# Kernel optimization log

Measured on AMD Instinct MI355X. Metric: run time of the kernel, lower is better.

Reference implementation:

```python
import jax, jax.numpy as jnp
import numpy as np

# Dims per init_kwargs
B, C_IN, H, W = 64, 512, 28, 28
GROWTH, BN_SIZE = 32, 4
C_MID = BN_SIZE * GROWTH  # 128
EPS = 1e-5
NUM_BITS = 8          # activation & weight quantization bits
NUM_CHUNKS = 16       # RangeBN chunking (eladhoffer quantize.py default)


def quantize(x, num_bits):
    """Uniform min/max quantize-dequantize (UniformQuantize forward)."""
    mn = x.min()
    mx = x.max()
    qmax = 2.0 ** num_bits - 1.0
    scale = jnp.maximum((mx - mn) / qmax, 1e-8)
    q = jnp.round((jnp.clip(x, mn, mx) - mn) / scale)
    return q * scale + mn


def conv2d(x, w, pad):
    return jax.lax.conv_general_dilated(
        x, w, window_strides=(1, 1), padding=[(pad, pad), (pad, pad)],
        dimension_numbers=('NCHW', 'OIHW', 'NCHW'))


def batchnorm2d(x, w, b):
    # training-mode BN: batch statistics over (N,H,W), biased variance
    mean = x.mean(axis=(0, 2, 3), keepdims=True)
    var = x.var(axis=(0, 2, 3), keepdims=True)
    xhat = (x - mean) * jax.lax.rsqrt(var + EPS)
    return xhat * w.reshape(1, -1, 1, 1) + b.reshape(1, -1, 1, 1)


def range_bn(x, w, b):
    # Range-based BN (training-mode): per-channel mean, scale from chunked min/max range
    Bx, Cx, Hx, Wx = x.shape
    y = x.transpose(1, 0, 2, 3).reshape(Cx, NUM_CHUNKS, -1)  # [C, chunks, n]
    mean_max = y.max(-1).mean(-1)   # [C]
    mean_min = y.min(-1).mean(-1)   # [C]
    mean = y.reshape(Cx, -1).mean(-1)  # [C]
    n = y.shape[-1]
    scale_fix = (0.5 * 0.35) * (1.0 + (np.pi * np.log(4.0)) ** 0.5) / ((2.0 * np.log(float(n))) ** 0.5)
    scale = 1.0 / ((mean_max - mean_min) * scale_fix + EPS)
    out = (x - mean.reshape(1, Cx, 1, 1)) * scale.reshape(1, Cx, 1, 1)
    qw = quantize(w, NUM_BITS)
    qb = quantize(b, NUM_BITS)
    return out * qw.reshape(1, Cx, 1, 1) + qb.reshape(1, Cx, 1, 1)


def setup_inputs() -> dict:
    key = jax.random.key(0)
    ks = jax.random.split(key, 7)
    x = jax.random.normal(ks[0], (B, C_IN, H, W), dtype=jnp.float32)
    bn1_w = jax.random.uniform(ks[1], (C_IN,), dtype=jnp.float32, minval=0.5, maxval=1.5)
    bn1_b = jax.random.normal(ks[2], (C_IN,), dtype=jnp.float32) * 0.1
    conv1_w = jax.random.normal(ks[3], (C_MID, C_IN, 1, 1), dtype=jnp.float32) * (2.0 / C_IN) ** 0.5
    rbn_w = jax.random.uniform(ks[4], (C_MID,), dtype=jnp.float32, minval=0.5, maxval=1.5)
    rbn_b = jax.random.normal(ks[5], (C_MID,), dtype=jnp.float32) * 0.1
    conv2_w = jax.random.normal(ks[6], (GROWTH, C_MID, 3, 3), dtype=jnp.float32) * (2.0 / (9 * C_MID)) ** 0.5
    return {"x": x, "bn1_w": bn1_w, "bn1_b": bn1_b, "conv1_w": conv1_w,
            "rbn_w": rbn_w, "rbn_b": rbn_b, "conv2_w": conv2_w}


def reference(x, bn1_w, bn1_b, conv1_w, rbn_w, rbn_b, conv2_w):
    # norm1 -> relu1 -> QConv2d(1x1) -> RangeBN -> relu2 -> QConv2d(3x3) -> concat
    h = jax.nn.relu(batchnorm2d(x, bn1_w, bn1_b))
    h = conv2d(quantize(h, NUM_BITS), quantize(conv1_w, NUM_BITS), pad=0)
    h = jax.nn.relu(range_bn(h, rbn_w, rbn_b))
    h = conv2d(quantize(h, NUM_BITS), quantize(conv2_w, NUM_BITS), pad=1)
    # drop_rate = 0 -> dropout is identity
    return jnp.concatenate([x, h], axis=1)
```

## Files before the change

kernel.cpp:

```cpp
#include <hip/hip_runtime.h>
#include <math.h>

static constexpr int BB    = 64;
static constexpr int C_IN  = 512;
static constexpr int C_MID = 128;
static constexpr int C_OUT = 32;
static constexpr int C_TOT = 544;
static constexpr int HW    = 784;

static constexpr size_t H2_OFF    = 0;
static constexpr size_t QW1_OFF   = 6422528;
static constexpr size_t QW2_OFF   = QW1_OFF + 65536;
static constexpr size_t PSTAT_OFF = QW2_OFF + 49152;
static constexpr size_t BNA_OFF   = PSTAT_OFF + 16384;
static constexpr size_t BNB_OFF   = BNA_OFF + 512;
static constexpr size_t A2_OFF    = BNB_OFF + 512;
static constexpr size_t B2_OFF    = A2_OFF + 128;
static constexpr size_t QRW_OFF   = B2_OFF + 128;
static constexpr size_t QRB_OFF   = QRW_OFF + 128;
static constexpr size_t SCAL_OFF  = QRB_OFF + 128;
static constexpr size_t ACELL_OFF = SCAL_OFF + 16;
static constexpr size_t RP_OFF    = ACELL_OFF + 112;

#define DEVFN __device__ __forceinline__

typedef __bf16 bf16x8 __attribute__((ext_vector_type(8)));
typedef float  f32x4  __attribute__((ext_vector_type(4)));

DEVFN float qact(float v, float mn, float mx, float inv, float sc) {
    v = fminf(fmaxf(v, mn), mx);
    return fmaf(rintf((v - mn) * inv), sc, mn);
}

DEVFN unsigned f2bf(float f) {
    unsigned u = __float_as_uint(f);
    return (u + 0x7fffu + ((u >> 16) & 1u)) >> 16;
}

DEVFN unsigned fkey(float f) {
    const unsigned u = __float_as_uint(f);
    return (u & 0x80000000u) ? ~u : (u | 0x80000000u);
}
DEVFN float funkey(unsigned k) {
    const unsigned u = (k & 0x80000000u) ? (k & 0x7FFFFFFFu) : ~k;
    return __uint_as_float(u);
}

__global__ void k_init(float* __restrict__ ws) {
    unsigned* cells = (unsigned*)(ws + ACELL_OFF);
    const int t = threadIdx.x;
    if (t < 3) cells[t] = 0xFFFFFFFFu;
    else if (t < 6) cells[4 + (t - 3)] = 0u;
}

__global__ __launch_bounds__(256) void k_stats(const float* __restrict__ x,
                                               const float* __restrict__ conv1_w,
                                               const float* __restrict__ conv2_w,
                                               float* __restrict__ ws) {
    const int bid = blockIdx.x, tid = threadIdx.x;
    __shared__ float r0[256], r1[256], r2[256], r3[256];

    if (bid < 4096) {
        const int c = bid >> 3, bg = bid & 7;
        float s = 0.f, s2 = 0.f, mn = INFINITY, mx = -INFINITY;
        if (tid < 224) {
#pragma unroll
            for (int k = 0; k < 7; ++k) {
                const int idx = k * 224 + tid;
                const int b = bg * 8 + idx / 196, j = idx % 196;
                const float4 v = ((const float4*)(x + ((size_t)b * C_IN + c) * HW))[j];
                s  += (v.x + v.y) + (v.z + v.w);
                s2 += v.x * v.x + v.y * v.y + v.z * v.z + v.w * v.w;
                mn = fminf(mn, fminf(fminf(v.x, v.y), fminf(v.z, v.w)));
                mx = fmaxf(mx, fmaxf(fmaxf(v.x, v.y), fmaxf(v.z, v.w)));
            }
        }
        r0[tid] = s; r1[tid] = s2; r2[tid] = mn; r3[tid] = mx;
        __syncthreads();
        for (int off = 128; off > 0; off >>= 1) {
            if (tid < off) {
                r0[tid] += r0[tid + off];
                r1[tid] += r1[tid + off];
                r2[tid] = fminf(r2[tid], r2[tid + off]);
                r3[tid] = fmaxf(r3[tid], r3[tid + off]);
            }
            __syncthreads();
        }
        if (tid == 0) {
            float* p = ws + PSTAT_OFF + ((size_t)c * 8 + bg) * 4;
            p[0] = r0[0]; p[1] = r1[0]; p[2] = r2[0]; p[3] = r3[0];
        }
    } else {
        float mn = INFINITY, mx = -INFINITY;
        if (bid < 4128) {
            const float4* src = (const float4*)conv1_w + (size_t)(bid - 4096) * 512;
            for (int i = tid; i < 512; i += 256) {
                const float4 v = src[i];
                mn = fminf(mn, fminf(fminf(v.x, v.y), fminf(v.z, v.w)));
                mx = fmaxf(mx, fmaxf(fmaxf(v.x, v.y), fmaxf(v.z, v.w)));
            }
        } else {
            const float4* src = (const float4*)conv2_w + (size_t)(bid - 4128) * 1152;
            for (int i = tid; i < 1152; i += 256) {
                const float4 v = src[i];
                mn = fminf(mn, fminf(fminf(v.x, v.y), fminf(v.z, v.w)));
                mx = fmaxf(mx, fmaxf(fmaxf(v.x, v.y), fmaxf(v.z, v.w)));
            }
        }
        r2[tid] = mn; r3[tid] = mx;
        __syncthreads();
        for (int off = 128; off > 0; off >>= 1) {
            if (tid < off) { r2[tid] = fminf(r2[tid], r2[tid + off]); r3[tid] = fmaxf(r3[tid], r3[tid + off]); }
            __syncthreads();
        }
        if (tid == 0) {
            unsigned* cells = (unsigned*)(ws + ACELL_OFF);
            const int w = (bid < 4128) ? 0 : 1;
            atomicMin(&cells[w],     fkey(r2[0]));
            atomicMax(&cells[4 + w], fkey(r3[0]));
        }
    }
}

__global__ __launch_bounds__(256) void k_prep(const float* __restrict__ conv1_w,
                                              const float* __restrict__ conv2_w,
                                              const float* __restrict__ bn1_w,
                                              const float* __restrict__ bn1_b,
                                              const float* __restrict__ rbn_w,
                                              const float* __restrict__ rbn_b,
                                              float* __restrict__ ws) {
    const int b = blockIdx.x, tid = threadIdx.x;
    const unsigned* cells = (const unsigned*)(ws + ACELL_OFF);
    __shared__ float ra[256], rb[256];
    __shared__ float s_mn, s_sc;

    if (b < 32) {
        const float mnw = funkey(cells[0]), mxw = funkey(cells[4]);
        const float scw = fmaxf((mxw - mnw) / 255.f, 1e-8f);
        unsigned short* qw = (unsigned short*)(ws + QW1_OFF);
        const int base = b * 2048;
#pragma unroll
        for (int t = 0; t < 8; ++t) {
            const int i = base + t * 256 + tid;
            const int co = i >> 9, k = i & 511;
            const float v = conv1_w[i];
            const float qv = fmaf(rintf((v - mnw) / scw), scw, mnw);
            const int ks = k >> 6, kc = (k >> 3) & 7, klo = k & 7;
            qw[(((size_t)ks * 128 + co) << 6) + (((kc ^ (co & 7)) << 3) | klo)] = (unsigned short)f2bf(qv);
        }
    } else if (b < 40) {
        const float mnw = funkey(cells[1]), mxw = funkey(cells[5]);
        const float scw = fmaxf((mxw - mnw) / 255.f, 1e-8f);
        unsigned short* qw2 = (unsigned short*)(ws + QW2_OFF);
        const int base = (b - 32) * 4608;
        for (int i2 = tid; i2 < 4608; i2 += 256) {
            const int i = base + i2;
            const int co = i / 1152, r = i % 1152, ci = r / 9, tap = r % 9;
            const float v = conv2_w[i];
            const float qv = fmaf(rintf((v - mnw) / scw), scw, mnw);
            qw2[(size_t)co * 1152 + tap * 128 + ci] = (unsigned short)f2bf(qv);
        }
    } else if (b == 40) {
        float lmn = INFINITY, lmx = -INFINITY;
        for (int c = tid; c < 512; c += 256) {
            const float* p = ws + PSTAT_OFF + (size_t)c * 32;
            float s = 0.f, s2 = 0.f, cmn = INFINITY, cmx = -INFINITY;
            for (int g = 0; g < 8; ++g) {
                s += p[g * 4 + 0]; s2 += p[g * 4 + 1];
                cmn = fminf(cmn, p[g * 4 + 2]); cmx = fmaxf(cmx, p[g * 4 + 3]);
            }
            const float n = 50176.f;
            const float mean = s / n;
            const float var  = s2 / n - mean * mean;
            const float rstd = rsqrtf(var + 1e-5f);
            const float A  = rstd * bn1_w[c];
            const float Bc = bn1_b[c] - mean * A;
            ws[BNA_OFF + c] = A; ws[BNB_OFF + c] = Bc;
            const float v1 = A * cmn + Bc, v2 = A * cmx + Bc;
            lmn = fminf(lmn, fmaxf(0.f, fminf(v1, v2)));
            lmx = fmaxf(lmx, fmaxf(0.f, fmaxf(v1, v2)));
        }
        ra[tid] = lmn; rb[tid] = lmx;
        __syncthreads();
        for (int off = 128; off > 0; off >>= 1) {
            if (tid < off) { ra[tid] = fminf(ra[tid], ra[tid + off]); rb[tid] = fmaxf(rb[tid], rb[tid + off]); }
            __syncthreads();
        }
        if (tid == 0) {
            const float mn1 = ra[0], mx1 = rb[0];
            const float sc = fmaxf((mx1 - mn1) / 255.f, 1e-8f);
            ws[SCAL_OFF + 0] = mn1; ws[SCAL_OFF + 1] = sc; ws[SCAL_OFF + 2] = 1.f / sc; ws[SCAL_OFF + 6] = mx1;
        }
    } else {
        for (int which = 0; which < 2; ++which) {
            const float* src = which ? rbn_b : rbn_w;
            const size_t dst = which ? QRB_OFF : QRW_OFF;
            float v = 0.f;
            ra[tid] = INFINITY; rb[tid] = -INFINITY;
            if (tid < 128) { v = src[tid]; ra[tid] = v; rb[tid] = v; }
            __syncthreads();
            for (int off = 128; off > 0; off >>= 1) {
                if (tid < off) { ra[tid] = fminf(ra[tid], ra[tid + off]); rb[tid] = fmaxf(rb[tid], rb[tid + off]); }
                __syncthreads();
            }
            if (tid == 0) { s_mn = ra[0]; s_sc = fmaxf((rb[0] - ra[0]) / 255.f, 1e-8f); }
            __syncthreads();
            if (tid < 128) ws[dst + tid] = fmaf(rintf((v - s_mn) / s_sc), s_sc, s_mn);
            __syncthreads();
        }
    }
}

__global__ __launch_bounds__(256, 2) void k_conv1(const float* __restrict__ x,
                                                  float* __restrict__ out,
                                                  float* __restrict__ ws) {
    __shared__ __align__(16) unsigned short wt[128 * 64];
    __shared__ __align__(16) unsigned short ht[112 * 64];
    const int tid = threadIdx.x;
    const int pt = blockIdx.x, b = blockIdx.y;
    const int p0 = pt * 112;
    const float mn1 = ws[SCAL_OFF + 0], sc1 = ws[SCAL_OFF + 1];
    const float inv1 = ws[SCAL_OFF + 2], mx1 = ws[SCAL_OFF + 6];
    const unsigned short* qw1 = (const unsigned short*)(ws + QW1_OFF);
    const float* xb = x + (size_t)b * C_IN * HW;
    float* outb = out + (size_t)b * C_TOT * HW;

    const int o = tid & 7, q = tid >> 3;
    const int wv = tid >> 6, g = (tid >> 4) & 3, r4 = tid & 15;

    f32x4 acc[2][7];
#pragma unroll
    for (int i = 0; i < 2; ++i)
#pragma unroll
        for (int j = 0; j < 7; ++j) acc[i][j] = f32x4{0.f, 0.f, 0.f, 0.f};

    for (int ks = 0; ks < 8; ++ks) {
        const float4* wsrc = (const float4*)(qw1 + (size_t)ks * 8192);
        float4* wdst = (float4*)wt;
#pragma unroll
        for (int i = 0; i < 4; ++i) wdst[tid + i * 256] = wsrc[tid + i * 256];

        if (tid < 224) {
            const int ci0 = ks * 64 + o * 8;
            float vv[8][4];
#pragma unroll
            for (int j = 0; j < 8; ++j) {
                const f32x4 v = *(const f32x4*)(xb + (size_t)(ci0 + j) * HW + p0 + q * 4);
                __builtin_nontemporal_store(v, (f32x4*)(outb + (size_t)(ci0 + j) * HW + p0 + q * 4));
                const float A = ws[BNA_OFF + ci0 + j], Bc = ws[BNB_OFF + ci0 + j];
                vv[j][0] = qact(fmaxf(0.f, fmaf(v.x, A, Bc)), mn1, mx1, inv1, sc1);
                vv[j][1] = qact(fmaxf(0.f, fmaf(v.y, A, Bc)), mn1, mx1, inv1, sc1);
                vv[j][2] = qact(fmaxf(0.f, fmaf(v.z, A, Bc)), mn1, mx1, inv1, sc1);
                vv[j][3] = qact(fmaxf(0.f, fmaf(v.w, A, Bc)), mn1, mx1, inv1, sc1);
            }
#pragma unroll
            for (int r = 0; r < 4; ++r) {
                const int p = q * 4 + r;
                uint4 pk;
                pk.x = f2bf(vv[0][r]) | (f2bf(vv[1][r]) << 16);
                pk.y = f2bf(vv[2][r]) | (f2bf(vv[3][r]) << 16);
                pk.z = f2bf(vv[4][r]) | (f2bf(vv[5][r]) << 16);
                pk.w = f2bf(vv[6][r]) | (f2bf(vv[7][r]) << 16);
                *(uint4*)&ht[p * 64 + ((o ^ (p & 7)) << 3)] = pk;
            }
        }
        __syncthreads();

#pragma unroll
        for (int ksub = 0; ksub < 2; ++ksub) {
            const int kk = ksub * 4 + g;
            bf16x8 af[2], bfr[7];
#pragma unroll
            for (int ct = 0; ct < 2; ++ct) {
                const int co = wv * 32 + ct * 16 + r4;
                af[ct] = *(const bf16x8*)&wt[co * 64 + ((kk ^ (co & 7)) << 3)];
            }
#pragma unroll
            for (int pf = 0; pf < 7; ++pf) {
                const int p = pf * 16 + r4;
                bfr[pf] = *(const bf16x8*)&ht[p * 64 + ((kk ^ (p & 7)) << 3)];
            }
#pragma unroll
            for (int ct = 0; ct < 2; ++ct)
#pragma unroll
                for (int pf = 0; pf < 7; ++pf)
                    acc[ct][pf] = __builtin_amdgcn_mfma_f32_16x16x32_bf16(af[ct], bfr[pf], acc[ct][pf], 0, 0, 0);
        }
        __syncthreads();
    }

    float* hb = ws + H2_OFF + (size_t)b * C_MID * HW;
#pragma unroll
    for (int ct = 0; ct < 2; ++ct) {
        const int co0 = wv * 32 + ct * 16 + g * 4;
#pragma unroll
        for (int pf = 0; pf < 7; ++pf) {
            const int p = p0 + pf * 16 + r4;
#pragma unroll
            for (int r = 0; r < 4; ++r)
                hb[(size_t)(co0 + r) * HW + p] = acc[ct][pf][r];
        }
    }

#pragma unroll
    for (int ct = 0; ct < 2; ++ct)
#pragma unroll
        for (int r = 0; r < 4; ++r) {
            float s = 0.f, mn = INFINITY, mx = -INFINITY;
#pragma unroll
            for (int pf = 0; pf < 7; ++pf) {
                const float v = acc[ct][pf][r];
                s += v; mn = fminf(mn, v); mx = fmaxf(mx, v);
            }
#pragma unroll
            for (int m = 1; m < 16; m <<= 1) {
                s  += __shfl_xor(s, m, 64);
                mn  = fminf(mn, __shfl_xor(mn, m, 64));
                mx  = fmaxf(mx, __shfl_xor(mx, m, 64));
            }
            if (r4 == 0) {
                const int co = wv * 32 + ct * 16 + g * 4 + r;
                float* dst = ws + RP_OFF + (((size_t)co * 64 + b) * 7 + pt) * 3;
                dst[0] = s; dst[1] = mn; dst[2] = mx;
            }
        }
}

__global__ __launch_bounds__(64) void k_rbn_combine(float* __restrict__ ws) {
    const int c = blockIdx.x, t = threadIdx.x;
    const int ch = t >> 2, sub = t & 3;
    const int b = ch * 4 + sub;
    const float* rp = ws + RP_OFF + ((size_t)c * 64 + b) * 21;
    float s = 0.f, mn = INFINITY, mx = -INFINITY;
#pragma unroll
    for (int pt = 0; pt < 7; ++pt) {
        s += rp[pt * 3 + 0];
        mn = fminf(mn, rp[pt * 3 + 1]);
        mx = fmaxf(mx, rp[pt * 3 + 2]);
    }
#pragma unroll
    for (int m = 1; m < 4; m <<= 1) {
        s  += __shfl_xor(s, m, 64);
        mn  = fminf(mn, __shfl_xor(mn, m, 64));
        mx  = fmaxf(mx, __shfl_xor(mx, m, 64));
    }
    float smx = mx, smn = mn, stot = s, gmn = mn, gmx = mx;
#pragma unroll
    for (int m = 4; m < 64; m <<= 1) {
        smx  += __shfl_xor(smx, m, 64);
        smn  += __shfl_xor(smn, m, 64);
        stot += __shfl_xor(stot, m, 64);
        gmn   = fminf(gmn, __shfl_xor(gmn, m, 64));
        gmx   = fmaxf(gmx, __shfl_xor(gmx, m, 64));
    }
    if (t == 0) {
        const float mm = smx * (1.f / 16.f), mnm = smn * (1.f / 16.f);
        const float mean = stot / 50176.f;
        const double PI_D = 3.14159265358979323846;
        const double sfd = 0.175 * (1.0 + sqrt(PI_D * log(4.0))) / sqrt(2.0 * log(3136.0));
        const float scale = 1.f / ((mm - mnm) * (float)sfd + 1e-5f);
        const float A  = scale * ws[QRW_OFF + c];
        const float Bc = ws[QRB_OFF + c] - mean * A;
        ws[A2_OFF + c] = A; ws[B2_OFF + c] = Bc;
        const float v1 = A * gmn + Bc, v2 = A * gmx + Bc;
        const float lo = fmaxf(0.f, fminf(v1, v2));
        const float hi = fmaxf(0.f, fmaxf(v1, v2));
        unsigned* cells = (unsigned*)(ws + ACELL_OFF);
        atomicMin(&cells[2], __float_as_uint(lo));
        atomicMax(&cells[6], __float_as_uint(hi));
    }
}

__global__ __launch_bounds__(128) void k_conv2(float* __restrict__ out, const float* __restrict__ ws) {
    __shared__ __align__(16) unsigned short lact[7 * 30 * 128];
    const int tid = threadIdx.x;
    const int pt = blockIdx.x, b = blockIdx.y;
    const int y0 = pt * 4;
    const unsigned* cells = (const unsigned*)(ws + ACELL_OFF);
    const float mn3 = __uint_as_float(cells[2]);
    const float mx3 = __uint_as_float(cells[6]);
    const float sc3 = fmaxf((mx3 - mn3) / 255.f, 1e-8f);
    const float inv3 = 1.f / sc3;

    {
        const uint4 z = {0u, 0u, 0u, 0u};
        uint4* lp = (uint4*)lact;
        for (int i = tid; i < 3360; i += 128) lp[i] = z;
    }
    __syncthreads();

    const float* h2b = ws + H2_OFF + (size_t)b * C_MID * HW;
    for (int task = tid; task < 672; task += 128) {
        const int oct = task / 42, rem = task % 42, r = rem / 7, xq = rem % 7;
        const int gy = y0 - 1 + r;
        if (gy < 0 || gy > 27) continue;
        float vv[8][4];
#pragma unroll
        for (int j = 0; j < 8; ++j) {
            const int ci = oct * 8 + j;
            const float4 v = *(const float4*)(h2b + (size_t)ci * HW + gy * 28 + xq * 4);
            const float A = ws[A2_OFF + ci], Bc = ws[B2_OFF + ci];
            vv[j][0] = qact(fmaxf(0.f, fmaf(v.x, A, Bc)), mn3, mx3, inv3, sc3);
            vv[j][1] = qact(fmaxf(0.f, fmaf(v.y, A, Bc)), mn3, mx3, inv3, sc3);
            vv[j][2] = qact(fmaxf(0.f, fmaf(v.z, A, Bc)), mn3, mx3, inv3, sc3);
            vv[j][3] = qact(fmaxf(0.f, fmaf(v.w, A, Bc)), mn3, mx3, inv3, sc3);
        }
#pragma unroll
        for (int xi = 0; xi < 4; ++xi) {
            const int col = xq * 4 + xi + 1;
            const int phys = (oct + col) & 15;
            uint4 pk;
            pk.x = f2bf(vv[0][xi]) | (f2bf(vv[1][xi]) << 16);
            pk.y = f2bf(vv[2][xi]) | (f2bf(vv[3][xi]) << 16);
            pk.z = f2bf(vv[4][xi]) | (f2bf(vv[5][xi]) << 16);
            pk.w = f2bf(vv[6][xi]) | (f2bf(vv[7][xi]) << 16);
            *(uint4*)&lact[((r * 30 + col) * 16 + phys) * 8] = pk;
        }
    }
    __syncthreads();

    const int wv = tid >> 6, lane = tid & 63, r4 = lane & 15, g = lane >> 4;
    int py[4], px[4];
#pragma unroll
    for (int i = 0; i < 4; ++i) {
        const int p = (wv * 4 + i) * 16 + r4;
        py[i] = p / 28; px[i] = p % 28;
    }
    f32x4 acc[2][4];
#pragma unroll
    for (int ct = 0; ct < 2; ++ct)
#pragma unroll
        for (int i = 0; i < 4; ++i) acc[ct][i] = f32x4{0.f, 0.f, 0.f, 0.f};

    const unsigned short* qw2 = (const unsigned short*)(ws + QW2_OFF);
    for (int tap = 0; tap < 9; ++tap) {
        const int dy = tap / 3, dx = tap % 3;
        bf16x8 afr[2][4];
#pragma unroll
        for (int ct = 0; ct < 2; ++ct)
#pragma unroll
            for (int c4 = 0; c4 < 4; ++c4) {
                const int co = ct * 16 + r4;
                afr[ct][c4] = *(const bf16x8*)&qw2[(size_t)co * 1152 + tap * 128 + c4 * 32 + g * 8];
            }
#pragma unroll
        for (int c4 = 0; c4 < 4; ++c4) {
            bf16x8 bfr[4];
#pragma unroll
            for (int i = 0; i < 4; ++i) {
                const int row = py[i] + dy, col = px[i] + dx;
                const int phys = (c4 * 4 + g + col) & 15;
                bfr[i] = *(const bf16x8*)&lact[((row * 30 + col) * 16 + phys) * 8];
            }
#pragma unroll
            for (int ct = 0; ct < 2; ++ct)
#pragma unroll
                for (int i = 0; i < 4; ++i)
                    acc[ct][i] = __builtin_amdgcn_mfma_f32_16x16x32_bf16(afr[ct][c4], bfr[i], acc[ct][i], 0, 0, 0);
        }
    }

#pragma unroll
    for (int ct = 0; ct < 2; ++ct)
#pragma unroll
        for (int i = 0; i < 4; ++i) {
            const int pf = wv * 4 + i;
            if (pf < 7) {
                const int p = pf * 16 + r4;
#pragma unroll
                for (int r = 0; r < 4; ++r) {
                    const int co = ct * 16 + g * 4 + r;
                    out[((size_t)b * C_TOT + 512 + co) * HW + y0 * 28 + p] = acc[ct][i][r];
                }
            }
        }
}

extern "C" void kernel_launch(void* const* d_in, const int* in_sizes, int n_in,
                              void* d_out, int out_size, void* d_ws, size_t ws_size,
                              hipStream_t stream) {
    const float* x       = (const float*)d_in[0];
    const float* bn1_w   = (const float*)d_in[1];
    const float* bn1_b   = (const float*)d_in[2];
    const float* conv1_w = (const float*)d_in[3];
    const float* rbn_w   = (const float*)d_in[4];
    const float* rbn_b   = (const float*)d_in[5];
    const float* conv2_w = (const float*)d_in[6];
    float* out = (float*)d_out;
    float* ws  = (float*)d_ws;

    k_init<<<1, 64, 0, stream>>>(ws);
    k_stats<<<4136, 256, 0, stream>>>(x, conv1_w, conv2_w, ws);
    k_prep<<<42, 256, 0, stream>>>(conv1_w, conv2_w, bn1_w, bn1_b, rbn_w, rbn_b, ws);
    k_conv1<<<dim3(7, 64), 256, 0, stream>>>(x, out, ws);
    k_rbn_combine<<<128, 64, 0, stream>>>(ws);
    k_conv2<<<dim3(7, 64), 128, 0, stream>>>(out, ws);
}
```

Baseline: 102.2 us.

## Split conv1 over output-channel halves, store h2 as bf16, drop atomics and init kernel

Replaces the atomic min/max cells and the k_init launch with per-block partial results that are reduced inside k_prep and k_conv2. conv1 is split into two blocks per tile, each covering 64 output channels, which gives more blocks and higher occupancy. Each of those blocks stages x and recomputes the BN/quantize of its input, and only one of them writes the x passthrough. The intermediate h2 is stored in bf16 instead of fp32, halving its write and read traffic at some precision cost before RangeBN. conv2 moves to 256 threads with fewer tiles per wave.

```diff
diff --git a/kernel.cpp b/kernel.cpp
--- a/kernel.cpp
+++ b/kernel.cpp
@@ -19,8 +19,9 @@
 static constexpr size_t QRW_OFF   = B2_OFF + 128;
 static constexpr size_t QRB_OFF   = QRW_OFF + 128;
 static constexpr size_t SCAL_OFF  = QRB_OFF + 128;
-static constexpr size_t ACELL_OFF = SCAL_OFF + 16;
-static constexpr size_t RP_OFF    = ACELL_OFF + 112;
+static constexpr size_t PART_OFF  = SCAL_OFF + 16;
+static constexpr size_t RP_OFF    = PART_OFF + 128;
+static constexpr size_t PART2_OFF = RP_OFF + 172032;
 
 #define DEVFN __device__ __forceinline__
 
@@ -37,21 +38,7 @@
     return (u + 0x7fffu + ((u >> 16) & 1u)) >> 16;
 }
 
-DEVFN unsigned fkey(float f) {
-    const unsigned u = __float_as_uint(f);
-    return (u & 0x80000000u) ? ~u : (u | 0x80000000u);
-}
-DEVFN float funkey(unsigned k) {
-    const unsigned u = (k & 0x80000000u) ? (k & 0x7FFFFFFFu) : ~k;
-    return __uint_as_float(u);
-}
-
-__global__ void k_init(float* __restrict__ ws) {
-    unsigned* cells = (unsigned*)(ws + ACELL_OFF);
-    const int t = threadIdx.x;
-    if (t < 3) cells[t] = 0xFFFFFFFFu;
-    else if (t < 6) cells[4 + (t - 3)] = 0u;
-}
+DEVFN float bf2f(unsigned short h) { return __uint_as_float((unsigned)h << 16); }
 
 __global__ __launch_bounds__(256) void k_stats(const float* __restrict__ x,
                                                const float* __restrict__ conv1_w,
@@ -63,17 +50,13 @@
     if (bid < 4096) {
         const int c = bid >> 3, bg = bid & 7;
         float s = 0.f, s2 = 0.f, mn = INFINITY, mx = -INFINITY;
-        if (tid < 224) {
-#pragma unroll
-            for (int k = 0; k < 7; ++k) {
-                const int idx = k * 224 + tid;
-                const int b = bg * 8 + idx / 196, j = idx % 196;
-                const float4 v = ((const float4*)(x + ((size_t)b * C_IN + c) * HW))[j];
-                s  += (v.x + v.y) + (v.z + v.w);
-                s2 += v.x * v.x + v.y * v.y + v.z * v.z + v.w * v.w;
-                mn = fminf(mn, fminf(fminf(v.x, v.y), fminf(v.z, v.w)));
-                mx = fmaxf(mx, fmaxf(fmaxf(v.x, v.y), fmaxf(v.z, v.w)));
-            }
+        for (int i = tid; i < 1568; i += 256) {
+            const int b = bg * 8 + i / 196, j = i % 196;
+            const float4 v = ((const float4*)(x + ((size_t)b * C_IN + c) * HW))[j];
+            s  += (v.x + v.y) + (v.z + v.w);
+            s2 += v.x * v.x + v.y * v.y + v.z * v.z + v.w * v.w;
+            mn = fminf(mn, fminf(fminf(v.x, v.y), fminf(v.z, v.w)));
+            mx = fmaxf(mx, fmaxf(fmaxf(v.x, v.y), fmaxf(v.z, v.w)));
         }
         r0[tid] = s; r1[tid] = s2; r2[tid] = mn; r3[tid] = mx;
         __syncthreads();
@@ -114,10 +97,9 @@
             __syncthreads();
         }
         if (tid == 0) {
-            unsigned* cells = (unsigned*)(ws + ACELL_OFF);
-            const int w = (bid < 4128) ? 0 : 1;
-            atomicMin(&cells[w],     fkey(r2[0]));
-            atomicMax(&cells[4 + w], fkey(r3[0]));
+            float* p = (bid < 4128) ? ws + PART_OFF + (size_t)(bid - 4096) * 2
+                                    : ws + PART_OFF + 64 + (size_t)(bid - 4128) * 2;
+            p[0] = r2[0]; p[1] = r3[0];
         }
     }
 }
@@ -130,13 +112,20 @@
                                               const float* __restrict__ rbn_b,
                                               float* __restrict__ ws) {
     const int b = blockIdx.x, tid = threadIdx.x;
-    const unsigned* cells = (const unsigned*)(ws + ACELL_OFF);
     __shared__ float ra[256], rb[256];
     __shared__ float s_mn, s_sc;
 
     if (b < 32) {
-        const float mnw = funkey(cells[0]), mxw = funkey(cells[4]);
-        const float scw = fmaxf((mxw - mnw) / 255.f, 1e-8f);
+        ra[tid] = tid < 32 ? ws[PART_OFF + tid * 2] : INFINITY;
+        rb[tid] = tid < 32 ? ws[PART_OFF + tid * 2 + 1] : -INFINITY;
+        __syncthreads();
+        for (int off = 128; off > 0; off >>= 1) {
+            if (tid < off) { ra[tid] = fminf(ra[tid], ra[tid + off]); rb[tid] = fmaxf(rb[tid], rb[tid + off]); }
+            __syncthreads();
+        }
+        if (tid == 0) { s_mn = ra[0]; s_sc = fmaxf((rb[0] - ra[0]) / 255.f, 1e-8f); }
+        __syncthreads();
+        const float mnw = s_mn, scw = s_sc;
         unsigned short* qw = (unsigned short*)(ws + QW1_OFF);
         const int base = b * 2048;
 #pragma unroll
@@ -149,8 +138,16 @@
             qw[(((size_t)ks * 128 + co) << 6) + (((kc ^ (co & 7)) << 3) | klo)] = (unsigned short)f2bf(qv);
         }
     } else if (b < 40) {
-        const float mnw = funkey(cells[1]), mxw = funkey(cells[5]);
-        const float scw = fmaxf((mxw - mnw) / 255.f, 1e-8f);
+        ra[tid] = tid < 8 ? ws[PART_OFF + 64 + tid * 2] : INFINITY;
+        rb[tid] = tid < 8 ? ws[PART_OFF + 64 + tid * 2 + 1] : -INFINITY;
+        __syncthreads();
+        for (int off = 128; off > 0; off >>= 1) {
+            if (tid < off) { ra[tid] = fminf(ra[tid], ra[tid + off]); rb[tid] = fmaxf(rb[tid], rb[tid + off]); }
+            __syncthreads();
+        }
+        if (tid == 0) { s_mn = ra[0]; s_sc = fmaxf((rb[0] - ra[0]) / 255.f, 1e-8f); }
+        __syncthreads();
+        const float mnw = s_mn, scw = s_sc;
         unsigned short* qw2 = (unsigned short*)(ws + QW2_OFF);
         const int base = (b - 32) * 4608;
         for (int i2 = tid; i2 < 4608; i2 += 256) {
@@ -211,13 +208,13 @@
     }
 }
 
-__global__ __launch_bounds__(256, 2) void k_conv1(const float* __restrict__ x,
+__global__ __launch_bounds__(256, 3) void k_conv1(const float* __restrict__ x,
                                                   float* __restrict__ out,
                                                   float* __restrict__ ws) {
-    __shared__ __align__(16) unsigned short wt[128 * 64];
+    __shared__ __align__(16) unsigned short wt[64 * 64];
     __shared__ __align__(16) unsigned short ht[112 * 64];
     const int tid = threadIdx.x;
-    const int pt = blockIdx.x, b = blockIdx.y;
+    const int pt = blockIdx.x, b = blockIdx.y, ch = blockIdx.z;
     const int p0 = pt * 112;
     const float mn1 = ws[SCAL_OFF + 0], sc1 = ws[SCAL_OFF + 1];
     const float inv1 = ws[SCAL_OFF + 2], mx1 = ws[SCAL_OFF + 6];
@@ -228,17 +225,15 @@
     const int o = tid & 7, q = tid >> 3;
     const int wv = tid >> 6, g = (tid >> 4) & 3, r4 = tid & 15;
 
-    f32x4 acc[2][7];
-#pragma unroll
-    for (int i = 0; i < 2; ++i)
-#pragma unroll
-        for (int j = 0; j < 7; ++j) acc[i][j] = f32x4{0.f, 0.f, 0.f, 0.f};
+    f32x4 acc[7];
+#pragma unroll
+    for (int j = 0; j < 7; ++j) acc[j] = f32x4{0.f, 0.f, 0.f, 0.f};
 
     for (int ks = 0; ks < 8; ++ks) {
-        const float4* wsrc = (const float4*)(qw1 + (size_t)ks * 8192);
+        const float4* wsrc = (const float4*)(qw1 + (((size_t)ks * 128 + (size_t)ch * 64) << 6));
         float4* wdst = (float4*)wt;
-#pragma unroll
-        for (int i = 0; i < 4; ++i) wdst[tid + i * 256] = wsrc[tid + i * 256];
+        wdst[tid] = wsrc[tid];
+        wdst[tid + 256] = wsrc[tid + 256];
 
         if (tid < 224) {
             const int ci0 = ks * 64 + o * 8;
@@ -246,7 +241,8 @@
 #pragma unroll
             for (int j = 0; j < 8; ++j) {
                 const f32x4 v = *(const f32x4*)(xb + (size_t)(ci0 + j) * HW + p0 + q * 4);
-                __builtin_nontemporal_store(v, (f32x4*)(outb + (size_t)(ci0 + j) * HW + p0 + q * 4));
+                if (ch == 0)
+                    __builtin_nontemporal_store(v, (f32x4*)(outb + (size_t)(ci0 + j) * HW + p0 + q * 4));
                 const float A = ws[BNA_OFF + ci0 + j], Bc = ws[BNB_OFF + ci0 + j];
                 vv[j][0] = qact(fmaxf(0.f, fmaf(v.x, A, Bc)), mn1, mx1, inv1, sc1);
                 vv[j][1] = qact(fmaxf(0.f, fmaf(v.y, A, Bc)), mn1, mx1, inv1, sc1);
@@ -269,61 +265,51 @@
 #pragma unroll
         for (int ksub = 0; ksub < 2; ++ksub) {
             const int kk = ksub * 4 + g;
-            bf16x8 af[2], bfr[7];
-#pragma unroll
-            for (int ct = 0; ct < 2; ++ct) {
-                const int co = wv * 32 + ct * 16 + r4;
-                af[ct] = *(const bf16x8*)&wt[co * 64 + ((kk ^ (co & 7)) << 3)];
-            }
+            const int col = wv * 16 + r4;
+            const bf16x8 af = *(const bf16x8*)&wt[col * 64 + ((kk ^ (col & 7)) << 3)];
+            bf16x8 bfr[7];
 #pragma unroll
             for (int pf = 0; pf < 7; ++pf) {
                 const int p = pf * 16 + r4;
                 bfr[pf] = *(const bf16x8*)&ht[p * 64 + ((kk ^ (p & 7)) << 3)];
             }
 #pragma unroll
-            for (int ct = 0; ct < 2; ++ct)
-#pragma unroll
-                for (int pf = 0; pf < 7; ++pf)
-                    acc[ct][pf] = __builtin_amdgcn_mfma_f32_16x16x32_bf16(af[ct], bfr[pf], acc[ct][pf], 0, 0, 0);
-        }
-        __syncthreads();
-    }
-
-    float* hb = ws + H2_OFF + (size_t)b * C_MID * HW;
-#pragma unroll
-    for (int ct = 0; ct < 2; ++ct) {
-        const int co0 = wv * 32 + ct * 16 + g * 4;
+            for (int pf = 0; pf < 7; ++pf)
+                acc[pf] = __builtin_amdgcn_mfma_f32_16x16x32_bf16(af, bfr[pf], acc[pf], 0, 0, 0);
+        }
+        __syncthreads();
+    }
+
+    unsigned short* hb = (unsigned short*)(ws + H2_OFF) + (size_t)b * C_MID * HW;
+    const int co0 = ch * 64 + wv * 16 + g * 4;
+#pragma unroll
+    for (int pf = 0; pf < 7; ++pf) {
+        const int p = p0 + pf * 16 + r4;
+#pragma unroll
+        for (int r = 0; r < 4; ++r)
+            hb[(size_t)(co0 + r) * HW + p] = (unsigned short)f2bf(acc[pf][r]);
+    }
+
+#pragma unroll
+    for (int r = 0; r < 4; ++r) {
+        float s = 0.f, mn = INFINITY, mx = -INFINITY;
 #pragma unroll
         for (int pf = 0; pf < 7; ++pf) {
-            const int p = p0 + pf * 16 + r4;
-#pragma unroll
-            for (int r = 0; r < 4; ++r)
-                hb[(size_t)(co0 + r) * HW + p] = acc[ct][pf][r];
-        }
-    }
-
-#pragma unroll
-    for (int ct = 0; ct < 2; ++ct)
-#pragma unroll
-        for (int r = 0; r < 4; ++r) {
-            float s = 0.f, mn = INFINITY, mx = -INFINITY;
-#pragma unroll
-            for (int pf = 0; pf < 7; ++pf) {
-                const float v = acc[ct][pf][r];
-                s += v; mn = fminf(mn, v); mx = fmaxf(mx, v);
-            }
-#pragma unroll
-            for (int m = 1; m < 16; m <<= 1) {
-                s  += __shfl_xor(s, m, 64);
-                mn  = fminf(mn, __shfl_xor(mn, m, 64));
-                mx  = fmaxf(mx, __shfl_xor(mx, m, 64));
-            }
-            if (r4 == 0) {
-                const int co = wv * 32 + ct * 16 + g * 4 + r;
-                float* dst = ws + RP_OFF + (((size_t)co * 64 + b) * 7 + pt) * 3;
-                dst[0] = s; dst[1] = mn; dst[2] = mx;
-            }
-        }
+            const float v = acc[pf][r];
+            s += v; mn = fminf(mn, v); mx = fmaxf(mx, v);
+        }
+#pragma unroll
+        for (int m = 1; m < 16; m <<= 1) {
+            s  += __shfl_xor(s, m, 64);
+            mn  = fminf(mn, __shfl_xor(mn, m, 64));
+            mx  = fmaxf(mx, __shfl_xor(mx, m, 64));
+        }
+        if (r4 == 0) {
+            const int co = co0 + r;
+            float* dst = ws + RP_OFF + (((size_t)co * 64 + b) * 7 + pt) * 3;
+            dst[0] = s; dst[1] = mn; dst[2] = mx;
+        }
+    }
 }
 
 __global__ __launch_bounds__(64) void k_rbn_combine(float* __restrict__ ws) {
@@ -363,34 +349,40 @@
         const float Bc = ws[QRB_OFF + c] - mean * A;
         ws[A2_OFF + c] = A; ws[B2_OFF + c] = Bc;
         const float v1 = A * gmn + Bc, v2 = A * gmx + Bc;
-        const float lo = fmaxf(0.f, fminf(v1, v2));
-        const float hi = fmaxf(0.f, fmaxf(v1, v2));
-        unsigned* cells = (unsigned*)(ws + ACELL_OFF);
-        atomicMin(&cells[2], __float_as_uint(lo));
-        atomicMax(&cells[6], __float_as_uint(hi));
-    }
-}
-
-__global__ __launch_bounds__(128) void k_conv2(float* __restrict__ out, const float* __restrict__ ws) {
+        ws[PART2_OFF + c * 2 + 0] = fmaxf(0.f, fminf(v1, v2));
+        ws[PART2_OFF + c * 2 + 1] = fmaxf(0.f, fmaxf(v1, v2));
+    }
+}
+
+__global__ __launch_bounds__(256, 2) void k_conv2(float* __restrict__ out, const float* __restrict__ ws) {
     __shared__ __align__(16) unsigned short lact[7 * 30 * 128];
+    __shared__ float sra[128], srb[128];
+    __shared__ float s_mn3, s_mx3, s_sc3, s_inv3;
     const int tid = threadIdx.x;
     const int pt = blockIdx.x, b = blockIdx.y;
     const int y0 = pt * 4;
-    const unsigned* cells = (const unsigned*)(ws + ACELL_OFF);
-    const float mn3 = __uint_as_float(cells[2]);
-    const float mx3 = __uint_as_float(cells[6]);
-    const float sc3 = fmaxf((mx3 - mn3) / 255.f, 1e-8f);
-    const float inv3 = 1.f / sc3;
-
+
+    if (tid < 128) { sra[tid] = ws[PART2_OFF + tid * 2]; srb[tid] = ws[PART2_OFF + tid * 2 + 1]; }
+    __syncthreads();
+    for (int off = 64; off > 0; off >>= 1) {
+        if (tid < off) { sra[tid] = fminf(sra[tid], sra[tid + off]); srb[tid] = fmaxf(srb[tid], srb[tid + off]); }
+        __syncthreads();
+    }
+    if (tid == 0) {
+        const float mn3 = sra[0], mx3 = srb[0];
+        const float sc = fmaxf((mx3 - mn3) / 255.f, 1e-8f);
+        s_mn3 = mn3; s_mx3 = mx3; s_sc3 = sc; s_inv3 = 1.f / sc;
+    }
     {
         const uint4 z = {0u, 0u, 0u, 0u};
         uint4* lp = (uint4*)lact;
-        for (int i = tid; i < 3360; i += 128) lp[i] = z;
+        for (int i = tid; i < 3360; i += 256) lp[i] = z;
     }
     __syncthreads();
-
-    const float* h2b = ws + H2_OFF + (size_t)b * C_MID * HW;
-    for (int task = tid; task < 672; task += 128) {
+    const float mn3 = s_mn3, mx3 = s_mx3, sc3 = s_sc3, inv3 = s_inv3;
+
+    const unsigned short* h2b = (const unsigned short*)(ws + H2_OFF) + (size_t)b * C_MID * HW;
+    for (int task = tid; task < 672; task += 256) {
         const int oct = task / 42, rem = task % 42, r = rem / 7, xq = rem % 7;
         const int gy = y0 - 1 + r;
         if (gy < 0 || gy > 27) continue;
@@ -398,12 +390,12 @@
 #pragma unroll
         for (int j = 0; j < 8; ++j) {
             const int ci = oct * 8 + j;
-            const float4 v = *(const float4*)(h2b + (size_t)ci * HW + gy * 28 + xq * 4);
+            const ushort4 v = *(const ushort4*)(h2b + (size_t)ci * HW + gy * 28 + xq * 4);
             const float A = ws[A2_OFF + ci], Bc = ws[B2_OFF + ci];
-            vv[j][0] = qact(fmaxf(0.f, fmaf(v.x, A, Bc)), mn3, mx3, inv3, sc3);
-            vv[j][1] = qact(fmaxf(0.f, fmaf(v.y, A, Bc)), mn3, mx3, inv3, sc3);
-            vv[j][2] = qact(fmaxf(0.f, fmaf(v.z, A, Bc)), mn3, mx3, inv3, sc3);
-            vv[j][3] = qact(fmaxf(0.f, fmaf(v.w, A, Bc)), mn3, mx3, inv3, sc3);
+            vv[j][0] = qact(fmaxf(0.f, fmaf(bf2f(v.x), A, Bc)), mn3, mx3, inv3, sc3);
+            vv[j][1] = qact(fmaxf(0.f, fmaf(bf2f(v.y), A, Bc)), mn3, mx3, inv3, sc3);
+            vv[j][2] = qact(fmaxf(0.f, fmaf(bf2f(v.z), A, Bc)), mn3, mx3, inv3, sc3);
+            vv[j][3] = qact(fmaxf(0.f, fmaf(bf2f(v.w), A, Bc)), mn3, mx3, inv3, sc3);
         }
 #pragma unroll
         for (int xi = 0; xi < 4; ++xi) {
@@ -420,17 +412,17 @@
     __syncthreads();
 
     const int wv = tid >> 6, lane = tid & 63, r4 = lane & 15, g = lane >> 4;
-    int py[4], px[4];
-#pragma unroll
-    for (int i = 0; i < 4; ++i) {
-        const int p = (wv * 4 + i) * 16 + r4;
+    int py[2], px[2];
+#pragma unroll
+    for (int i = 0; i < 2; ++i) {
+        const int p = (wv * 2 + i) * 16 + r4;
         py[i] = p / 28; px[i] = p % 28;
     }
-    f32x4 acc[2][4];
+    f32x4 acc[2][2];
 #pragma unroll
     for (int ct = 0; ct < 2; ++ct)
 #pragma unroll
-        for (int i = 0; i < 4; ++i) acc[ct][i] = f32x4{0.f, 0.f, 0.f, 0.f};
+        for (int i = 0; i < 2; ++i) acc[ct][i] = f32x4{0.f, 0.f, 0.f, 0.f};
 
     const unsigned short* qw2 = (const unsigned short*)(ws + QW2_OFF);
     for (int tap = 0; tap < 9; ++tap) {
@@ -445,9 +437,9 @@
             }
 #pragma unroll
         for (int c4 = 0; c4 < 4; ++c4) {
-            bf16x8 bfr[4];
-#pragma unroll
-            for (int i = 0; i < 4; ++i) {
+            bf16x8 bfr[2];
+#pragma unroll
+            for (int i = 0; i < 2; ++i) {
                 const int row = py[i] + dy, col = px[i] + dx;
                 const int phys = (c4 * 4 + g + col) & 15;
                 bfr[i] = *(const bf16x8*)&lact[((row * 30 + col) * 16 + phys) * 8];
@@ -455,7 +447,7 @@
 #pragma unroll
             for (int ct = 0; ct < 2; ++ct)
 #pragma unroll
-                for (int i = 0; i < 4; ++i)
+                for (int i = 0; i < 2; ++i)
                     acc[ct][i] = __builtin_amdgcn_mfma_f32_16x16x32_bf16(afr[ct][c4], bfr[i], acc[ct][i], 0, 0, 0);
         }
     }
@@ -463,8 +455,8 @@
 #pragma unroll
     for (int ct = 0; ct < 2; ++ct)
 #pragma unroll
-        for (int i = 0; i < 4; ++i) {
-            const int pf = wv * 4 + i;
+        for (int i = 0; i < 2; ++i) {
+            const int pf = wv * 2 + i;
             if (pf < 7) {
                 const int p = pf * 16 + r4;
 #pragma unroll
@@ -489,10 +481,9 @@
     float* out = (float*)d_out;
     float* ws  = (float*)d_ws;
 
-    k_init<<<1, 64, 0, stream>>>(ws);
     k_stats<<<4136, 256, 0, stream>>>(x, conv1_w, conv2_w, ws);
     k_prep<<<42, 256, 0, stream>>>(conv1_w, conv2_w, bn1_w, bn1_b, rbn_w, rbn_b, ws);
-    k_conv1<<<dim3(7, 64), 256, 0, stream>>>(x, out, ws);
+    k_conv1<<<dim3(7, 64, 2), 256, 0, stream>>>(x, out, ws);
     k_rbn_combine<<<128, 64, 0, stream>>>(ws);
-    k_conv2<<<dim3(7, 64), 128, 0, stream>>>(out, ws);
-}
+    k_conv2<<<dim3(7, 64), 256, 0, stream>>>(out, ws);
+}
```

After: 123.7 us. 21.0% more time.
